# Performance work log

Measured on AMD Instinct MI355X. Metric: run time of the kernel, lower is better.

## Reference

```python
import jax, jax.numpy as jnp
import numpy as np

N = 8388608
HID = 8
P = 10.0
EPS = 1e-8
LR = 1.0
EXP_P = float(np.exp(np.float32(P)))  # exp(10) ~ 22026.466


def setup_inputs() -> dict:
    key = jax.random.key(0)
    ks = jax.random.split(key, 12)
    s = 0.3
    inp = {
        "h": jnp.zeros((N, HID), jnp.float32),
        "g": jax.random.normal(ks[0], (N,), jnp.float32),
        # GRUCell params (flax: input denses no bias, hidden denses with bias)
        "Wi_r": jax.random.normal(ks[1], (2, HID), jnp.float32) * s,
        "Wh_r": jax.random.normal(ks[2], (HID, HID), jnp.float32) * s,
        "bh_r": jax.random.normal(ks[3], (HID,), jnp.float32) * s,
        "Wi_z": jax.random.normal(ks[4], (2, HID), jnp.float32) * s,
        "Wh_z": jax.random.normal(ks[5], (HID, HID), jnp.float32) * s,
        "bh_z": jax.random.normal(ks[6], (HID,), jnp.float32) * s,
        "Wi_n": jax.random.normal(ks[7], (2, HID), jnp.float32) * s,
        "Wh_n": jax.random.normal(ks[8], (HID, HID), jnp.float32) * s,
        "bh_n": jax.random.normal(ks[9], (HID,), jnp.float32) * s,
        # MLP: single Dense(1) (mlp_dims=(), trailing relu popped)
        "Wm": jax.random.normal(ks[10], (HID, 1), jnp.float32) * s,
        "bm": jax.random.normal(ks[11], (1,), jnp.float32) * s,
    }
    return inp


def reference(h, g, Wi_r, Wh_r, bh_r, Wi_z, Wh_z, bh_z, Wi_n, Wh_n, bh_n, Wm, bm):
    g2 = jax.lax.stop_gradient(g[..., None])            # [N,1]
    g_sign = jnp.sign(g2)
    g_log = jnp.log(jnp.abs(g2) + EPS) / P              # [N,1]
    g_in1 = jnp.concatenate([g_log, g_sign], axis=-1)   # [N,2]
    g_in2 = jnp.concatenate([-jnp.ones_like(g2), EXP_P * g2], axis=-1)
    g_in = jnp.where(g_log >= -1.0, g_in1, g_in2)       # [N,2] (broadcast select)

    # flax GRUCell: r,z gates sigmoid, candidate tanh, input dense has no bias
    r = jax.nn.sigmoid(g_in @ Wi_r + h @ Wh_r + bh_r)
    z = jax.nn.sigmoid(g_in @ Wi_z + h @ Wh_z + bh_z)
    n = jnp.tanh(g_in @ Wi_n + r * (h @ Wh_n + bh_n))
    h_new = (1.0 - z) * n + z * h                        # [N,8]

    outs = h_new @ Wm + bm                               # [N,1]
    out = -LR * jnp.exp(outs) * g2                       # [N,1]
    return h_new, out[..., 0]
```

## Files before the change

kernel.cpp:

```cpp
#include <hip/hip_runtime.h>


typedef float f32x2 __attribute__((ext_vector_type(2)));

#define SWZ(x, imm) __int_as_float(__builtin_amdgcn_ds_swizzle(__float_as_int(x), (imm)))
#define PIN(x) asm volatile("" : "+v"(x))

#define PK_FMA_BLO(d, a, bp) \
    asm("v_pk_fma_f32 %0, %1, %2, %0 op_sel:[0,0,0] op_sel_hi:[1,0,1]" \
        : "+v"(d) : "v"(a), "v"(bp))
#define PK_FMA_BHI(d, a, bp) \
    asm("v_pk_fma_f32 %0, %1, %2, %0 op_sel:[0,1,0] op_sel_hi:[1,1,1]" \
        : "+v"(d) : "v"(a), "v"(bp))
#define PK_FMA3_BLO(d, a, bp, c) \
    asm("v_pk_fma_f32 %0, %1, %2, %3 op_sel:[0,0,0] op_sel_hi:[1,0,1]" \
        : "=v"(d) : "v"(a), "v"(bp), "v"(c))
#define PK_MUL_BLO(d, a, bp) \
    asm("v_pk_mul_f32 %0, %1, %2 op_sel:[0,0] op_sel_hi:[1,0]" \
        : "=v"(d) : "v"(a), "v"(bp))

__global__ __launch_bounds__(256, 4) void gru_l2l_kernel(
    const float* __restrict__ hp, const float* __restrict__ gp,
    const float* __restrict__ Wi_r, const float* __restrict__ Wh_r, const float* __restrict__ bh_r,
    const float* __restrict__ Wi_z, const float* __restrict__ Wh_z, const float* __restrict__ bh_z,
    const float* __restrict__ Wi_n, const float* __restrict__ Wh_n, const float* __restrict__ bh_n,
    const float* __restrict__ Wm, const float* __restrict__ bm,
    float* __restrict__ out, int nrows)
{
    const int npairs = nrows << 2;
    const int tid    = blockIdx.x * blockDim.x + threadIdx.x;
    const int stride = blockDim.x * gridDim.x;
    const int m      = tid & 3;
    const int c0     = m << 1;

    const float L2E = 1.44269504088896341f;

    f32x2 wir0 = { Wi_r[c0] * L2E,     Wi_r[c0 + 1] * L2E };
    f32x2 wir1 = { Wi_r[8 + c0] * L2E, Wi_r[8 + c0 + 1] * L2E };
    f32x2 wiz0 = { Wi_z[c0] * L2E,     Wi_z[c0 + 1] * L2E };
    f32x2 wiz1 = { Wi_z[8 + c0] * L2E, Wi_z[8 + c0 + 1] * L2E };
    f32x2 win0 = { Wi_n[c0],           Wi_n[c0 + 1] };
    f32x2 win1 = { Wi_n[8 + c0],       Wi_n[8 + c0 + 1] };
    f32x2 whr[8], whz[8], whn[8];
#pragma unroll
    for (int k = 0; k < 8; ++k) {
        whr[k] = (f32x2){ Wh_r[k * 8 + c0] * L2E, Wh_r[k * 8 + c0 + 1] * L2E };
        whz[k] = (f32x2){ Wh_z[k * 8 + c0] * L2E, Wh_z[k * 8 + c0 + 1] * L2E };
        whn[k] = (f32x2){ Wh_n[k * 8 + c0],       Wh_n[k * 8 + c0 + 1] };
    }
    f32x2 br = { bh_r[c0] * L2E, bh_r[c0 + 1] * L2E };
    f32x2 bz = { bh_z[c0] * L2E, bh_z[c0 + 1] * L2E };
    f32x2 bn = { bh_n[c0],       bh_n[c0 + 1] };
    float wmx  = Wm[c0], wmy = Wm[c0 + 1];
    float bmv2 = bm[0] * L2E;

    PIN(wir0); PIN(wir1); PIN(wiz0); PIN(wiz1); PIN(win0); PIN(win1);
#pragma unroll
    for (int k = 0; k < 8; ++k) { PIN(whr[k]); PIN(whz[k]); PIN(whn[k]); }
    PIN(br); PIN(bz); PIN(bn); PIN(wmx); PIN(wmy); PIN(bmv2);
    asm volatile("" ::: "memory");

    const f32x2* __restrict__ hp2  = (const f32x2*)hp;
    f32x2* __restrict__       out2 = (f32x2*)out;
    float* __restrict__       outo = out + ((long)nrows << 3);

    for (int p = tid; p < npairs; p += stride) {
        const int   row = p >> 2;
        f32x2       hv  = hp2[p];
        const float g   = gp[row];

        const float ag = fabsf(g) + 1e-8f;
        const float lg = __builtin_amdgcn_logf(ag) * 0.069314718055994531f;
        f32x2 gin;
        if (lg >= -1.0f) {
            gin.x = lg;
            gin.y = (g > 0.0f) ? 1.0f : -1.0f;
        } else {
            gin.x = -1.0f;
            gin.y = 22026.465794806718f * g;
        }

        f32x2 hb0, hb1, hb2, hb3;
        hb0.x = SWZ(hv.x, 0x01C); hb0.y = SWZ(hv.y, 0x01C);
        hb1.x = SWZ(hv.x, 0x03C); hb1.y = SWZ(hv.y, 0x03C);
        hb2.x = SWZ(hv.x, 0x05C); hb2.y = SWZ(hv.y, 0x05C);
        hb3.x = SWZ(hv.x, 0x07C); hb3.y = SWZ(hv.y, 0x07C);

        f32x2 ar, az, an, hn;
        PK_FMA3_BLO(ar, wir0, gin, br);
        PK_FMA_BHI (ar, wir1, gin);
        PK_FMA3_BLO(az, wiz0, gin, bz);
        PK_FMA_BHI (az, wiz1, gin);
        PK_MUL_BLO (an, win0, gin);
        PK_FMA_BHI (an, win1, gin);
        PK_FMA3_BLO(hn, whn[0], hb0, bn);
        PK_FMA_BLO (ar, whr[0], hb0);
        PK_FMA_BLO (az, whz[0], hb0);
        PK_FMA_BHI (ar, whr[1], hb0);
        PK_FMA_BHI (az, whz[1], hb0);
        PK_FMA_BHI (hn, whn[1], hb0);
#define DOT2(Q, K0, K1) \
        PK_FMA_BLO(ar, whr[K0], hb##Q); \
        PK_FMA_BLO(az, whz[K0], hb##Q); \
        PK_FMA_BLO(hn, whn[K0], hb##Q); \
        PK_FMA_BHI(ar, whr[K1], hb##Q); \
        PK_FMA_BHI(az, whz[K1], hb##Q); \
        PK_FMA_BHI(hn, whn[K1], hb##Q);
        DOT2(1, 2, 3) DOT2(2, 4, 5) DOT2(3, 6, 7)
#undef DOT2

        const float rx = __builtin_amdgcn_rcpf(1.0f + __builtin_amdgcn_exp2f(-ar.x));
        const float ry = __builtin_amdgcn_rcpf(1.0f + __builtin_amdgcn_exp2f(-ar.y));
        const float zx = __builtin_amdgcn_rcpf(1.0f + __builtin_amdgcn_exp2f(-az.x));
        const float zy = __builtin_amdgcn_rcpf(1.0f + __builtin_amdgcn_exp2f(-az.y));

        const float prex = fmaf(rx, hn.x, an.x);
        const float prey = fmaf(ry, hn.y, an.y);
        const float tx = __builtin_amdgcn_exp2f(-2.885390081777927f * fabsf(prex));
        const float ty = __builtin_amdgcn_exp2f(-2.885390081777927f * fabsf(prey));
        const float nx = copysignf((1.0f - tx) * __builtin_amdgcn_rcpf(1.0f + tx), prex);
        const float ny = copysignf((1.0f - ty) * __builtin_amdgcn_rcpf(1.0f + ty), prey);
        const float hnx = fmaf(zx, hv.x - nx, nx);
        const float hny = fmaf(zy, hv.y - ny, ny);
        f32x2 ho; ho.x = hnx; ho.y = hny;
        out2[p] = ho;

        float s = fmaf(hny, wmy, hnx * wmx);
        s += SWZ(s, 0x041F);
        s += SWZ(s, 0x081F);
        if (m == 0) {
            outo[row] = -__builtin_amdgcn_exp2f(fmaf(s, L2E, bmv2)) * g;
        }
    }
}

extern "C" void kernel_launch(void* const* d_in, const int* in_sizes, int n_in,
                              void* d_out, int out_size, void* d_ws, size_t ws_size,
                              hipStream_t stream) {
    const float* hp   = (const float*)d_in[0];
    const float* gp   = (const float*)d_in[1];
    const float* Wi_r = (const float*)d_in[2];
    const float* Wh_r = (const float*)d_in[3];
    const float* bh_r = (const float*)d_in[4];
    const float* Wi_z = (const float*)d_in[5];
    const float* Wh_z = (const float*)d_in[6];
    const float* bh_z = (const float*)d_in[7];
    const float* Wi_n = (const float*)d_in[8];
    const float* Wh_n = (const float*)d_in[9];
    const float* bh_n = (const float*)d_in[10];
    const float* Wm   = (const float*)d_in[11];
    const float* bm   = (const float*)d_in[12];
    const int nrows   = in_sizes[1];

    gru_l2l_kernel<<<8192, 256, 0, stream>>>(hp, gp, Wi_r, Wh_r, bh_r,
                                             Wi_z, Wh_z, bh_z,
                                             Wi_n, Wh_n, bh_n,
                                             Wm, bm, (float*)d_out, nrows);
}
```

Baseline: 566.8 us.

## Replace ds_swizzle with DPP quad-perm broadcasts and unroll grid-stride loop by two

Swaps the LDS-based ds_swizzle lane exchanges for DPP quad_perm moves, which run in the VALU without LDS round trips or waitcnts. The grid-stride loop is unrolled by two, issuing both iterations' loads before compute to raise memory-level parallelism, and the gin branch becomes selects. This adds register pressure under launch_bounds(256,4), and a tail path handles the odd leftover iteration.

```diff
diff --git a/kernel.cpp b/kernel.cpp
--- a/kernel.cpp
+++ b/kernel.cpp
@@ -3,8 +3,15 @@
 
 typedef float f32x2 __attribute__((ext_vector_type(2)));
 
-#define SWZ(x, imm) __int_as_float(__builtin_amdgcn_ds_swizzle(__float_as_int(x), (imm)))
 #define PIN(x) asm volatile("" : "+v"(x))
+
+#define QP(x, ctrl) __int_as_float(__builtin_amdgcn_mov_dpp(__float_as_int(x), (ctrl), 0xF, 0xF, false))
+#define QP_B0 0x00
+#define QP_B1 0x55
+#define QP_B2 0xAA
+#define QP_B3 0xFF
+#define QP_X1 0xB1
+#define QP_X2 0x4E
 
 #define PK_FMA_BLO(d, a, bp) \
     asm("v_pk_fma_f32 %0, %1, %2, %0 op_sel:[0,0,0] op_sel_hi:[1,0,1]" \
@@ -64,27 +71,20 @@
     f32x2* __restrict__       out2 = (f32x2*)out;
     float* __restrict__       outo = out + ((long)nrows << 3);
 
-    for (int p = tid; p < npairs; p += stride) {
-        const int   row = p >> 2;
-        f32x2       hv  = hp2[p];
-        const float g   = gp[row];
-
+    auto body = [&](const f32x2 hv, const float g, const int p) -> float {
         const float ag = fabsf(g) + 1e-8f;
         const float lg = __builtin_amdgcn_logf(ag) * 0.069314718055994531f;
+        const bool  hi = (lg >= -1.0f);
         f32x2 gin;
-        if (lg >= -1.0f) {
-            gin.x = lg;
-            gin.y = (g > 0.0f) ? 1.0f : -1.0f;
-        } else {
-            gin.x = -1.0f;
-            gin.y = 22026.465794806718f * g;
-        }
+        gin.x = hi ? lg : -1.0f;
+        gin.y = hi ? ((g > 0.0f) ? 1.0f : -1.0f)
+                   : 22026.465794806718f * g;
 
         f32x2 hb0, hb1, hb2, hb3;
-        hb0.x = SWZ(hv.x, 0x01C); hb0.y = SWZ(hv.y, 0x01C);
-        hb1.x = SWZ(hv.x, 0x03C); hb1.y = SWZ(hv.y, 0x03C);
-        hb2.x = SWZ(hv.x, 0x05C); hb2.y = SWZ(hv.y, 0x05C);
-        hb3.x = SWZ(hv.x, 0x07C); hb3.y = SWZ(hv.y, 0x07C);
+        hb0.x = QP(hv.x, QP_B0); hb0.y = QP(hv.y, QP_B0);
+        hb1.x = QP(hv.x, QP_B1); hb1.y = QP(hv.y, QP_B1);
+        hb2.x = QP(hv.x, QP_B2); hb2.y = QP(hv.y, QP_B2);
+        hb3.x = QP(hv.x, QP_B3); hb3.y = QP(hv.y, QP_B3);
 
         f32x2 ar, az, an, hn;
         PK_FMA3_BLO(ar, wir0, gin, br);
@@ -126,10 +126,34 @@
         out2[p] = ho;
 
         float s = fmaf(hny, wmy, hnx * wmx);
-        s += SWZ(s, 0x041F);
-        s += SWZ(s, 0x081F);
+        s += QP(s, QP_X1);
+        s += QP(s, QP_X2);
+        return s;
+    };
+
+    const int stride2 = stride << 1;
+    int p = tid;
+    for (; p + stride < npairs; p += stride2) {
+        const int pB = p + stride;
+        const f32x2 hvA = hp2[p];
+        const float gA  = gp[p >> 2];
+        const f32x2 hvB = hp2[pB];
+        const float gB  = gp[pB >> 2];
+
+        const float sA = body(hvA, gA, p);
+        const float sB = body(hvB, gB, pB);
+
         if (m == 0) {
-            outo[row] = -__builtin_amdgcn_exp2f(fmaf(s, L2E, bmv2)) * g;
+            outo[p >> 2]  = -__builtin_amdgcn_exp2f(fmaf(sA, L2E, bmv2)) * gA;
+            outo[pB >> 2] = -__builtin_amdgcn_exp2f(fmaf(sB, L2E, bmv2)) * gB;
+        }
+    }
+    if (p < npairs) {
+        const f32x2 hv = hp2[p];
+        const float g  = gp[p >> 2];
+        const float s  = body(hv, g, p);
+        if (m == 0) {
+            outo[p >> 2] = -__builtin_amdgcn_exp2f(fmaf(s, L2E, bmv2)) * g;
         }
     }
 }
```

New measurement: 558.3 us. About the same (-1.5%).
